# Kernel optimization log

Hardware: AMD Instinct MI355X
Metric: run time of the kernel (lower is better)

## Reference

```python
import jax, jax.numpy as jnp
import numpy as np

SEQ_LEN = 1024
WINDOW = 32
NUM_HEADS = 16
BATCH = 8
DIM = 1024


def make_local_mask(seq_len=SEQ_LEN, window=WINDOW):
    # True = position is MASKED (disallowed), matching the torch bool attn_mask.
    # torch allows j in [i - window//2, i + window//2] inclusive.
    i = np.arange(seq_len)[:, None]
    j = np.arange(seq_len)[None, :]
    half = window // 2
    allowed = (j >= i - half) & (j <= i + half)
    return jnp.asarray(~allowed)


def setup_inputs() -> dict:
    key = jax.random.key(0)
    k_x, k_wi, k_wo = jax.random.split(key, 3)
    scale_in = 1.0 / np.sqrt(DIM)
    return {
        "x": jax.random.normal(k_x, (BATCH, SEQ_LEN, DIM), dtype=jnp.float32),
        "w_in": jax.random.normal(k_wi, (3 * DIM, DIM), dtype=jnp.float32) * scale_in,
        "b_in": jnp.zeros((3 * DIM,), dtype=jnp.float32),
        "w_out": jax.random.normal(k_wo, (DIM, DIM), dtype=jnp.float32) * scale_in,
        "b_out": jnp.zeros((DIM,), dtype=jnp.float32),
        "mask": make_local_mask(),
    }


def reference(x, w_in, b_in, w_out, b_out, mask):
    B, S, D = x.shape
    H = NUM_HEADS
    hd = D // H
    # fused in-projection (torch nn.MultiheadAttention self-attn path)
    qkv = x @ w_in.T + b_in                      # [B, S, 3D]
    q, k, v = jnp.split(qkv, 3, axis=-1)
    q = q.reshape(B, S, H, hd).transpose(0, 2, 1, 3)  # [B, H, S, hd]
    k = k.reshape(B, S, H, hd).transpose(0, 2, 1, 3)
    v = v.reshape(B, S, H, hd).transpose(0, 2, 1, 3)
    scores = jnp.einsum("bhqd,bhkd->bhqk", q, k) / jnp.sqrt(jnp.asarray(hd, x.dtype))
    neg = jnp.asarray(jnp.finfo(x.dtype).min, x.dtype)
    scores = jnp.where(mask[None, None, :, :], neg, scores)
    attn = jax.nn.softmax(scores, axis=-1)
    ctx = jnp.einsum("bhqk,bhkd->bhqd", attn, v)  # [B, H, S, hd]
    ctx = ctx.transpose(0, 2, 1, 3).reshape(B, S, D)
    return ctx @ w_out.T + b_out
```

## Files before the change

kernel.cpp:

```cpp
#include <hip/hip_runtime.h>

#define S_LEN   1024
#define NH      16
#define HD      64
#define BATCHN  8
#define DMODEL  1024
#define HALF_W  16

typedef __attribute__((ext_vector_type(8))) short bf16x8;
typedef __attribute__((ext_vector_type(4))) float f32x4;

__device__ __forceinline__ unsigned short f2bf(float f) {
  unsigned u = __builtin_bit_cast(unsigned, f);
  u += 0x7fffu + ((u >> 16) & 1u);
  return (unsigned short)(u >> 16);
}
__device__ __forceinline__ float bf2f(unsigned short h) {
  return __builtin_bit_cast(float, ((unsigned)h) << 16);
}

__device__ __forceinline__ void gload_lds16(const void* g, void* l) {
  __builtin_amdgcn_global_load_lds(
      (const __attribute__((address_space(1))) void*)g,
      (__attribute__((address_space(3))) void*)l, 16, 0, 0);
}

__global__ __launch_bounds__(256) void cvt_bf16_kernel(
    const float* __restrict__ in, unsigned short* __restrict__ out, int n4) {
  int t = blockIdx.x * 256 + threadIdx.x;
  if (t >= n4) return;
  float4 v = reinterpret_cast<const float4*>(in)[t];
  ushort4 o = make_ushort4(f2bf(v.x), f2bf(v.y), f2bf(v.z), f2bf(v.w));
  reinterpret_cast<ushort4*>(out)[t] = o;
}

#define MFMA_BF16 __builtin_amdgcn_mfma_f32_16x16x32_bf16

template <int OUT_BF16, int CHN>
__global__ __launch_bounds__(512, 2) void gemmdp_kernel(
    const unsigned short* __restrict__ A,
    const unsigned short* __restrict__ B,
    const float* __restrict__ bias,
    void* __restrict__ Cv,
    int N, int gy) {
  __shared__ __align__(16) unsigned short sA[2][2][CHN * 4096];
  __shared__ __align__(16) unsigned short sB[2][2][8192];

  const int tid  = threadIdx.x;
  const int lane = tid & 63;
  const int wid  = tid >> 6;
  const int wm   = wid >> 2;
  const int wn   = wid & 3;
  const int lgrp = lane >> 4;
  const int l15  = lane & 15;

  const int nwg = gridDim.x;
  const int cpx = nwg >> 3;
  const int sid = (blockIdx.x & 7) * cpx + (blockIdx.x >> 3);
  const int tileM = (sid / gy) * (CHN * 128);
  const int tileN = (sid % gy) * 256;

  const int srow = tid >> 2;
  const int scol = ((tid & 3) ^ ((tid >> 3) & 3)) * 8;
  const unsigned short* gA_s = A + (size_t)(tileM + srow) * 1024 + scol;
  const unsigned short* gB_s = B + (size_t)(tileN + srow) * 1024 + scol;

  const int fch  = (lgrp ^ ((l15 >> 1) & 3)) * 8;
  const int arow = (wm * (CHN * 64) + l15) * 32 + fch;
  const int brow = (wn * 64 + l15) * 32 + fch;

  f32x4 acc[CHN * 4][4] = {};
  bf16x8 nb0 = {}, nb1 = {}, nb2 = {}, nb3 = {};

#define SSA(KT, BUF, KH) do {                                              \
    const unsigned short* _sa = gA_s + (KT) * 64 + (KH) * 32;              \
    gload_lds16(_sa, &sA[BUF][KH][wid * 512]);                             \
    if constexpr (CHN == 2)                                                \
      gload_lds16(_sa + 131072, &sA[BUF][KH][4096 + wid * 512]);           \
  } while (0)
#define SSB(KT, BUF, KH) do {                                              \
    const unsigned short* _sb = gB_s + (KT) * 64 + (KH) * 32;              \
    gload_lds16(_sb, &sB[BUF][KH][wid * 512]);                             \
    gload_lds16(_sb + 131072, &sB[BUF][KH][4096 + wid * 512]);             \
  } while (0)

#define GATE_S do {                                                        \
    if constexpr (CHN == 2) asm volatile("s_waitcnt vmcnt(8)" ::: "memory");\
    else                    asm volatile("s_waitcnt vmcnt(6)" ::: "memory");\
    __builtin_amdgcn_sched_barrier(0);                                     \
    __builtin_amdgcn_s_barrier(); } while (0)
#define GATE_H do {                                                        \
    if constexpr (CHN == 2) asm volatile("s_waitcnt vmcnt(4)" ::: "memory");\
    else                    asm volatile("s_waitcnt vmcnt(3)" ::: "memory");\
    __builtin_amdgcn_sched_barrier(0);                                     \
    __builtin_amdgcn_s_barrier(); } while (0)
#define GATE_Z do {                                                        \
    asm volatile("s_waitcnt vmcnt(0)" ::: "memory");                       \
    __builtin_amdgcn_sched_barrier(0);                                     \
    __builtin_amdgcn_s_barrier(); } while (0)

#define PH(BUF, KH, CH, STG) do {                                          \
    const unsigned short* _pa = &sA[BUF][KH][arow + (CH) * 2048];          \
    bf16x8 a0_ = *(const bf16x8*)(_pa);                                    \
    bf16x8 a1_ = *(const bf16x8*)(_pa + 512);                              \
    bf16x8 a2_ = *(const bf16x8*)(_pa + 1024);                             \
    bf16x8 a3_ = *(const bf16x8*)(_pa + 1536);                             \
    if ((CH) == 0) {                                                       \
      const unsigned short* _pb = &sB[BUF][KH][brow];                      \
      nb0 = *(const bf16x8*)(_pb);        nb1 = *(const bf16x8*)(_pb + 512);  \
      nb2 = *(const bf16x8*)(_pb + 1024); nb3 = *(const bf16x8*)(_pb + 1536); } \
    STG;                                                                   \
    asm volatile("s_waitcnt lgkmcnt(0)" ::: "memory");                     \
    __builtin_amdgcn_sched_barrier(0);                                     \
    __builtin_amdgcn_s_setprio(1);                                         \
    acc[(CH)*4+0][0] = MFMA_BF16(a0_, nb0, acc[(CH)*4+0][0], 0, 0, 0);     \
    acc[(CH)*4+0][1] = MFMA_BF16(a0_, nb1, acc[(CH)*4+0][1], 0, 0, 0);     \
    acc[(CH)*4+0][2] = MFMA_BF16(a0_, nb2, acc[(CH)*4+0][2], 0, 0, 0);     \
    acc[(CH)*4+0][3] = MFMA_BF16(a0_, nb3, acc[(CH)*4+0][3], 0, 0, 0);     \
    acc[(CH)*4+1][0] = MFMA_BF16(a1_, nb0, acc[(CH)*4+1][0], 0, 0, 0);     \
    acc[(CH)*4+1][1] = MFMA_BF16(a1_, nb1, acc[(CH)*4+1][1], 0, 0, 0);     \
    acc[(CH)*4+1][2] = MFMA_BF16(a1_, nb2, acc[(CH)*4+1][2], 0, 0, 0);     \
    acc[(CH)*4+1][3] = MFMA_BF16(a1_, nb3, acc[(CH)*4+1][3], 0, 0, 0);     \
    acc[(CH)*4+2][0] = MFMA_BF16(a2_, nb0, acc[(CH)*4+2][0], 0, 0, 0);     \
    acc[(CH)*4+2][1] = MFMA_BF16(a2_, nb1, acc[(CH)*4+2][1], 0, 0, 0);     \
    acc[(CH)*4+2][2] = MFMA_BF16(a2_, nb2, acc[(CH)*4+2][2], 0, 0, 0);     \
    acc[(CH)*4+2][3] = MFMA_BF16(a2_, nb3, acc[(CH)*4+2][3], 0, 0, 0);     \
    acc[(CH)*4+3][0] = MFMA_BF16(a3_, nb0, acc[(CH)*4+3][0], 0, 0, 0);     \
    acc[(CH)*4+3][1] = MFMA_BF16(a3_, nb1, acc[(CH)*4+3][1], 0, 0, 0);     \
    acc[(CH)*4+3][2] = MFMA_BF16(a3_, nb2, acc[(CH)*4+3][2], 0, 0, 0);     \
    acc[(CH)*4+3][3] = MFMA_BF16(a3_, nb3, acc[(CH)*4+3][3], 0, 0, 0);     \
    __builtin_amdgcn_s_setprio(0);                                         \
  } while (0)

#define DOPAIR(BUF, KH, STGA, STGB) do {                                   \
    if constexpr (CHN == 2) {                                              \
      PH(BUF, KH, 0, STGA);                                                \
      PH(BUF, KH, 1, STGB);                                                \
    } else {                                                               \
      PH(BUF, KH, 0, do { STGA; STGB; } while (0));                        \
    } } while (0)
#define NOSTG ((void)0)

  SSA(0, 0, 0); SSB(0, 0, 0);
  SSA(0, 0, 1); SSB(0, 0, 1);
  SSA(1, 1, 0); SSB(1, 1, 0);

#pragma unroll 1
  for (int kt = 0; kt < 14; kt += 2) {
    GATE_S; DOPAIR(0, 0, SSA(kt + 1, 1, 1), SSB(kt + 1, 1, 1));
    GATE_S; DOPAIR(0, 1, SSA(kt + 2, 0, 0), SSB(kt + 2, 0, 0));
    GATE_S; DOPAIR(1, 0, SSA(kt + 2, 0, 1), SSB(kt + 2, 0, 1));
    GATE_S; DOPAIR(1, 1, SSA(kt + 3, 1, 0), SSB(kt + 3, 1, 0));
  }
  GATE_S; DOPAIR(0, 0, SSA(15, 1, 1), SSB(15, 1, 1));
  GATE_S; DOPAIR(0, 1, NOSTG, NOSTG);
  GATE_H; DOPAIR(1, 0, NOSTG, NOSTG);
  GATE_Z; DOPAIR(1, 1, NOSTG, NOSTG);

#undef SSA
#undef SSB
#undef GATE_S
#undef GATE_H
#undef GATE_Z
#undef PH
#undef DOPAIR
#undef NOSTG

#pragma unroll
  for (int nt = 0; nt < 4; ++nt) {
    const int col = tileN + wn * 64 + nt * 16 + l15;
    const float bs = bias[col];
#pragma unroll
    for (int ch = 0; ch < CHN; ++ch)
#pragma unroll
      for (int mt = 0; mt < 4; ++mt) {
        const int row0 = tileM + wm * (CHN * 64) + ch * 64 + mt * 16 + lgrp * 4;
#pragma unroll
        for (int rr = 0; rr < 4; ++rr) {
          float v = acc[ch * 4 + mt][nt][rr] + bs;
          if (OUT_BF16) {
            ((unsigned short*)Cv)[(size_t)(row0 + rr) * N + col] = f2bf(v);
          } else {
            ((float*)Cv)[(size_t)(row0 + rr) * N + col] = v;
          }
        }
      }
  }
}

#define KST 72
#define PST 104

__global__ __launch_bounds__(256) void attn_local_kernel(
    const unsigned short* __restrict__ qkv, unsigned short* __restrict__ ctx) {
  __shared__ __align__(16) unsigned short sKP[96 * KST];
  __shared__ __align__(16) unsigned short sQ[64 * KST];
  __shared__ __align__(16) unsigned short sVT[64 * PST];

  const int tid  = threadIdx.x;
  const int lane = tid & 63;
  const int wid  = tid >> 6;
  const int qc   = lane & 15;
  const int lgrp = lane >> 4;

  const int qb = blockIdx.x & 15;
  const int h  = (blockIdx.x >> 4) & 15;
  const int b  = blockIdx.x >> 8;
  const int i0 = qb * 64;

  const unsigned short* hb = qkv + (size_t)b * S_LEN * 3072 + (size_t)h * HD;

#pragma unroll
  for (int it = 0; it < 3; ++it) {
    int c  = it * 256 + tid;
    int r  = c >> 3;
    int d0 = (c & 7) * 8;
    int j  = i0 - 16 + r;
    bf16x8 kv = {}, vv = {};
    if (0 <= j && j < S_LEN) {
      const unsigned short* rp = hb + (size_t)j * 3072;
      kv = *reinterpret_cast<const bf16x8*>(rp + DMODEL + d0);
      vv = *reinterpret_cast<const bf16x8*>(rp + 2 * DMODEL + d0);
    }
    *reinterpret_cast<bf16x8*>(&sKP[r * KST + d0]) = kv;
#pragma unroll
    for (int jj = 0; jj < 8; ++jj) {
      int dd = (jj + c) & 7;
      sVT[(d0 + dd) * PST + r] = (unsigned short)vv[dd];
    }
  }
#pragma unroll
  for (int it = 0; it < 2; ++it) {
    int c  = it * 256 + tid;
    int r  = c >> 3;
    int d0 = (c & 7) * 8;
    bf16x8 qv = *reinterpret_cast<const bf16x8*>(hb + (size_t)(i0 + r) * 3072 + d0);
    *reinterpret_cast<bf16x8*>(&sQ[r * KST + d0]) = qv;
  }
  __syncthreads();

  const int q0 = wid * 16;

  bf16x8 bq[2];
#pragma unroll
  for (int ks = 0; ks < 2; ++ks)
    bq[ks] = *reinterpret_cast<const bf16x8*>(
        &sQ[(q0 + qc) * KST + ks * 32 + lgrp * 8]);

  f32x4 st[6] = {};
#pragma unroll
  for (int kt = 0; kt < 6; ++kt) {
#pragma unroll
    for (int ks = 0; ks < 2; ++ks) {
      bf16x8 fa = *reinterpret_cast<const bf16x8*>(
          &sKP[(kt * 16 + qc) * KST + ks * 32 + lgrp * 8]);
      st[kt] = __builtin_amdgcn_mfma_f32_16x16x32_bf16(fa, bq[ks], st[kt], 0, 0, 0);
    }
  }
  __syncthreads();

  const int q = q0 + qc;
  float pv[6][4];
  float mx = -3.0e38f;
#pragma unroll
  for (int kt = 0; kt < 6; ++kt)
#pragma unroll
    for (int rr = 0; rr < 4; ++rr) {
      int kk = kt * 16 + lgrp * 4 + rr;
      int j  = i0 - 16 + kk;
      bool ok = (j >= 0) && (j < S_LEN) && (kk >= q) && (kk <= q + 32);
      float s = ok ? st[kt][rr] * 0.125f : -3.0e38f;
      pv[kt][rr] = s;
      mx = fmaxf(mx, s);
    }
  mx = fmaxf(mx, __shfl_xor(mx, 16, 64));
  mx = fmaxf(mx, __shfl_xor(mx, 32, 64));

  float rsum = 0.f;
#pragma unroll
  for (int kt = 0; kt < 6; ++kt)
#pragma unroll
    for (int rr = 0; rr < 4; ++rr) {
      float p = __expf(pv[kt][rr] - mx);
      pv[kt][rr] = p;
      rsum += p;
    }
  rsum += __shfl_xor(rsum, 16, 64);
  rsum += __shfl_xor(rsum, 32, 64);
  const float inv = 1.0f / rsum;

  unsigned short* sP = sKP;
#pragma unroll
  for (int kt = 0; kt < 6; ++kt) {
    ushort4 w = make_ushort4(f2bf(pv[kt][0]), f2bf(pv[kt][1]),
                             f2bf(pv[kt][2]), f2bf(pv[kt][3]));
    *reinterpret_cast<ushort4*>(&sP[(q0 + qc) * PST + kt * 16 + lgrp * 4]) = w;
  }

  bf16x8 pb[3];
#pragma unroll
  for (int ks = 0; ks < 3; ++ks)
    pb[ks] = *reinterpret_cast<const bf16x8*>(
        &sP[(q0 + qc) * PST + ks * 32 + lgrp * 8]);

  f32x4 ct[4] = {};
#pragma unroll
  for (int dt = 0; dt < 4; ++dt)
#pragma unroll
    for (int ks = 0; ks < 3; ++ks) {
      bf16x8 fa = *reinterpret_cast<const bf16x8*>(
          &sVT[(dt * 16 + qc) * PST + ks * 32 + lgrp * 8]);
      ct[dt] = __builtin_amdgcn_mfma_f32_16x16x32_bf16(fa, pb[ks], ct[dt], 0, 0, 0);
    }

  unsigned short* op =
      ctx + ((size_t)b * S_LEN + i0 + q0 + qc) * DMODEL + h * HD;
#pragma unroll
  for (int dt = 0; dt < 4; ++dt) {
    ushort4 w = make_ushort4(
        f2bf(ct[dt][0] * inv), f2bf(ct[dt][1] * inv),
        f2bf(ct[dt][2] * inv), f2bf(ct[dt][3] * inv));
    *reinterpret_cast<ushort4*>(op + dt * 16 + lgrp * 4) = w;
  }
}

extern "C" void kernel_launch(void* const* d_in, const int* in_sizes, int n_in,
                              void* d_out, int out_size, void* d_ws, size_t ws_size,
                              hipStream_t stream) {
  const float* x     = (const float*)d_in[0];
  const float* w_in  = (const float*)d_in[1];
  const float* b_in  = (const float*)d_in[2];
  const float* w_out = (const float*)d_in[3];
  const float* b_out = (const float*)d_in[4];
  float* out = (float*)d_out;

  unsigned short* xb   = (unsigned short*)d_ws;
  unsigned short* wib  = xb  + (size_t)8192 * 1024;
  unsigned short* wob  = wib + (size_t)3072 * 1024;
  unsigned short* qkv  = wob + (size_t)1024 * 1024;
  unsigned short* ctxb = qkv + (size_t)8192 * 3072;

  cvt_bf16_kernel<<<8192, 256, 0, stream>>>(x, xb, (8192 * 1024) / 4);
  cvt_bf16_kernel<<<3072, 256, 0, stream>>>(w_in, wib, (3072 * 1024) / 4);
  cvt_bf16_kernel<<<1024, 256, 0, stream>>>(w_out, wob, (1024 * 1024) / 4);

  gemmdp_kernel<1, 2><<<384, 512, 0, stream>>>(
      xb, wib, b_in, (void*)qkv, 3072, 12);

  attn_local_kernel<<<BATCHN * NH * (S_LEN / 64), 256, 0, stream>>>(qkv, ctxb);

  gemmdp_kernel<0, 1><<<256, 512, 0, stream>>>(
      ctxb, wob, b_out, (void*)out, 1024, 4);
}
```

Baseline: 128.3 us.

## Retile QKV projection GEMM to 256x384 tiles with 4-stage LDS ring

The in-projection GEMM gets a dedicated kernel. Each workgroup computes a 256x384 tile, giving 256 workgroups (one per CU) instead of 384. K is streamed in 32-wide steps through a 4-slot LDS ring, with loads issued three steps ahead. This aims to remove the partial second wave and raise operand reuse per LDS load. In exchange it needs 48 accumulators per lane and 160KB of LDS, which limits occupancy and adds register pressure. The out-projection GEMM is specialised with its constants, with no structural change.

New measurement: 121.2 us. 5.6% less time.

```diff
diff --git a/kernel.cpp b/kernel.cpp
--- a/kernel.cpp
+++ b/kernel.cpp
@@ -36,15 +36,12 @@
 
 #define MFMA_BF16 __builtin_amdgcn_mfma_f32_16x16x32_bf16
 
-template <int OUT_BF16, int CHN>
-__global__ __launch_bounds__(512, 2) void gemmdp_kernel(
+__global__ __launch_bounds__(512, 2) void gemm_inproj_kernel(
     const unsigned short* __restrict__ A,
     const unsigned short* __restrict__ B,
     const float* __restrict__ bias,
-    void* __restrict__ Cv,
-    int N, int gy) {
-  __shared__ __align__(16) unsigned short sA[2][2][CHN * 4096];
-  __shared__ __align__(16) unsigned short sB[2][2][8192];
+    unsigned short* __restrict__ C) {
+  __shared__ __align__(16) unsigned short lds[81920];
 
   const int tid  = threadIdx.x;
   const int lane = tid & 63;
@@ -54,11 +51,9 @@
   const int lgrp = lane >> 4;
   const int l15  = lane & 15;
 
-  const int nwg = gridDim.x;
-  const int cpx = nwg >> 3;
-  const int sid = (blockIdx.x & 7) * cpx + (blockIdx.x >> 3);
-  const int tileM = (sid / gy) * (CHN * 128);
-  const int tileN = (sid % gy) * 256;
+  const int sid = (blockIdx.x & 7) * 32 + (blockIdx.x >> 3);
+  const int tileM = (sid >> 3) * 256;
+  const int tileN = (sid & 7) * 384;
 
   const int srow = tid >> 2;
   const int scol = ((tid & 3) ^ ((tid >> 3) & 3)) * 8;
@@ -66,79 +61,184 @@
   const unsigned short* gB_s = B + (size_t)(tileN + srow) * 1024 + scol;
 
   const int fch  = (lgrp ^ ((l15 >> 1) & 3)) * 8;
-  const int arow = (wm * (CHN * 64) + l15) * 32 + fch;
+  const int arow = (wm * 128 + l15) * 32 + fch;
+  const int brow = (wn * 96 + l15) * 32 + fch;
+
+  f32x4 acc[48] = {};
+
+#define STG(S) do { const int _q = (S) & 3;                                \
+    const unsigned short* _ga = gA_s + (S) * 32;                           \
+    const unsigned short* _gb = gB_s + (S) * 32;                           \
+    gload_lds16(_ga,          &lds[_q * 8192 + tid * 8]);                  \
+    gload_lds16(_ga + 131072, &lds[_q * 8192 + 4096 + tid * 8]);           \
+    gload_lds16(_gb,          &lds[32768 + _q * 12288 + tid * 8]);         \
+    gload_lds16(_gb + 131072, &lds[32768 + _q * 12288 + 4096 + tid * 8]);  \
+    gload_lds16(_gb + 262144, &lds[32768 + _q * 12288 + 8192 + tid * 8]);  \
+  } while (0)
+
+#define M24(MB)                                                            \
+    acc[(MB+0)*6+0] = MFMA_BF16(a0_, b0_, acc[(MB+0)*6+0], 0, 0, 0);       \
+    acc[(MB+0)*6+1] = MFMA_BF16(a0_, b1_, acc[(MB+0)*6+1], 0, 0, 0);       \
+    acc[(MB+0)*6+2] = MFMA_BF16(a0_, b2_, acc[(MB+0)*6+2], 0, 0, 0);       \
+    acc[(MB+0)*6+3] = MFMA_BF16(a0_, b3_, acc[(MB+0)*6+3], 0, 0, 0);       \
+    acc[(MB+0)*6+4] = MFMA_BF16(a0_, b4_, acc[(MB+0)*6+4], 0, 0, 0);       \
+    acc[(MB+0)*6+5] = MFMA_BF16(a0_, b5_, acc[(MB+0)*6+5], 0, 0, 0);       \
+    acc[(MB+1)*6+0] = MFMA_BF16(a1_, b0_, acc[(MB+1)*6+0], 0, 0, 0);       \
+    acc[(MB+1)*6+1] = MFMA_BF16(a1_, b1_, acc[(MB+1)*6+1], 0, 0, 0);       \
+    acc[(MB+1)*6+2] = MFMA_BF16(a1_, b2_, acc[(MB+1)*6+2], 0, 0, 0);       \
+    acc[(MB+1)*6+3] = MFMA_BF16(a1_, b3_, acc[(MB+1)*6+3], 0, 0, 0);       \
+    acc[(MB+1)*6+4] = MFMA_BF16(a1_, b4_, acc[(MB+1)*6+4], 0, 0, 0);       \
+    acc[(MB+1)*6+5] = MFMA_BF16(a1_, b5_, acc[(MB+1)*6+5], 0, 0, 0);       \
+    acc[(MB+2)*6+0] = MFMA_BF16(a2_, b0_, acc[(MB+2)*6+0], 0, 0, 0);       \
+    acc[(MB+2)*6+1] = MFMA_BF16(a2_, b1_, acc[(MB+2)*6+1], 0, 0, 0);       \
+    acc[(MB+2)*6+2] = MFMA_BF16(a2_, b2_, acc[(MB+2)*6+2], 0, 0, 0);       \
+    acc[(MB+2)*6+3] = MFMA_BF16(a2_, b3_, acc[(MB+2)*6+3], 0, 0, 0);       \
+    acc[(MB+2)*6+4] = MFMA_BF16(a2_, b4_, acc[(MB+2)*6+4], 0, 0, 0);       \
+    acc[(MB+2)*6+5] = MFMA_BF16(a2_, b5_, acc[(MB+2)*6+5], 0, 0, 0);       \
+    acc[(MB+3)*6+0] = MFMA_BF16(a3_, b0_, acc[(MB+3)*6+0], 0, 0, 0);       \
+    acc[(MB+3)*6+1] = MFMA_BF16(a3_, b1_, acc[(MB+3)*6+1], 0, 0, 0);       \
+    acc[(MB+3)*6+2] = MFMA_BF16(a3_, b2_, acc[(MB+3)*6+2], 0, 0, 0);       \
+    acc[(MB+3)*6+3] = MFMA_BF16(a3_, b3_, acc[(MB+3)*6+3], 0, 0, 0);       \
+    acc[(MB+3)*6+4] = MFMA_BF16(a3_, b4_, acc[(MB+3)*6+4], 0, 0, 0);       \
+    acc[(MB+3)*6+5] = MFMA_BF16(a3_, b5_, acc[(MB+3)*6+5], 0, 0, 0);
+
+  STG(0); STG(1); STG(2);
+
+#pragma unroll 1
+  for (int p = 0; p < 32; ++p) {
+    if (p < 30)       { asm volatile("s_waitcnt vmcnt(10)" ::: "memory"); }
+    else if (p == 30) { asm volatile("s_waitcnt vmcnt(5)"  ::: "memory"); }
+    else              { asm volatile("s_waitcnt vmcnt(0)"  ::: "memory"); }
+    __builtin_amdgcn_sched_barrier(0);
+    __builtin_amdgcn_s_barrier();
+
+    if (p <= 28) STG(p + 3);
+
+    const int slot = p & 3;
+    const unsigned short* pa = &lds[slot * 8192 + arow];
+    const unsigned short* pb = &lds[32768 + slot * 12288 + brow];
+
+    bf16x8 b0_ = *(const bf16x8*)(pb);
+    bf16x8 b1_ = *(const bf16x8*)(pb + 512);
+    bf16x8 b2_ = *(const bf16x8*)(pb + 1024);
+    bf16x8 b3_ = *(const bf16x8*)(pb + 1536);
+    bf16x8 b4_ = *(const bf16x8*)(pb + 2048);
+    bf16x8 b5_ = *(const bf16x8*)(pb + 2560);
+    bf16x8 a0_ = *(const bf16x8*)(pa);
+    bf16x8 a1_ = *(const bf16x8*)(pa + 512);
+    bf16x8 a2_ = *(const bf16x8*)(pa + 1024);
+    bf16x8 a3_ = *(const bf16x8*)(pa + 1536);
+    asm volatile("s_waitcnt lgkmcnt(0)" ::: "memory");
+    __builtin_amdgcn_sched_barrier(0);
+    __builtin_amdgcn_s_setprio(1);
+    M24(0)
+    __builtin_amdgcn_s_setprio(0);
+
+    a0_ = *(const bf16x8*)(pa + 2048);
+    a1_ = *(const bf16x8*)(pa + 2560);
+    a2_ = *(const bf16x8*)(pa + 3072);
+    a3_ = *(const bf16x8*)(pa + 3584);
+    asm volatile("s_waitcnt lgkmcnt(0)" ::: "memory");
+    __builtin_amdgcn_sched_barrier(0);
+    __builtin_amdgcn_s_setprio(1);
+    M24(4)
+    __builtin_amdgcn_s_setprio(0);
+  }
+#undef STG
+#undef M24
+
+#pragma unroll
+  for (int nt = 0; nt < 6; ++nt) {
+    const int col = tileN + wn * 96 + nt * 16 + l15;
+    const float bs = bias[col];
+#pragma unroll
+    for (int mt = 0; mt < 8; ++mt) {
+      const int row0 = tileM + wm * 128 + mt * 16 + lgrp * 4;
+#pragma unroll
+      for (int rr = 0; rr < 4; ++rr)
+        C[(size_t)(row0 + rr) * 3072 + col] = f2bf(acc[mt * 6 + nt][rr] + bs);
+    }
+  }
+}
+
+__global__ __launch_bounds__(512, 2) void gemm_outproj_kernel(
+    const unsigned short* __restrict__ A,
+    const unsigned short* __restrict__ B,
+    const float* __restrict__ bias,
+    float* __restrict__ Cv) {
+  __shared__ __align__(16) unsigned short sA[2][2][4096];
+  __shared__ __align__(16) unsigned short sB[2][2][8192];
+
+  const int tid  = threadIdx.x;
+  const int lane = tid & 63;
+  const int wid  = tid >> 6;
+  const int wm   = wid >> 2;
+  const int wn   = wid & 3;
+  const int lgrp = lane >> 4;
+  const int l15  = lane & 15;
+
+  const int sid = (blockIdx.x & 7) * 32 + (blockIdx.x >> 3);
+  const int tileM = (sid >> 2) * 128;
+  const int tileN = (sid & 3) * 256;
+
+  const int srow = tid >> 2;
+  const int scol = ((tid & 3) ^ ((tid >> 3) & 3)) * 8;
+  const unsigned short* gA_s = A + (size_t)(tileM + srow) * 1024 + scol;
+  const unsigned short* gB_s = B + (size_t)(tileN + srow) * 1024 + scol;
+
+  const int fch  = (lgrp ^ ((l15 >> 1) & 3)) * 8;
+  const int arow = (wm * 64 + l15) * 32 + fch;
   const int brow = (wn * 64 + l15) * 32 + fch;
 
-  f32x4 acc[CHN * 4][4] = {};
-  bf16x8 nb0 = {}, nb1 = {}, nb2 = {}, nb3 = {};
+  f32x4 acc[4][4] = {};
 
 #define SSA(KT, BUF, KH) do {                                              \
-    const unsigned short* _sa = gA_s + (KT) * 64 + (KH) * 32;              \
-    gload_lds16(_sa, &sA[BUF][KH][wid * 512]);                             \
-    if constexpr (CHN == 2)                                                \
-      gload_lds16(_sa + 131072, &sA[BUF][KH][4096 + wid * 512]);           \
+    gload_lds16(gA_s + (KT) * 64 + (KH) * 32, &sA[BUF][KH][wid * 512]);    \
   } while (0)
 #define SSB(KT, BUF, KH) do {                                              \
     const unsigned short* _sb = gB_s + (KT) * 64 + (KH) * 32;              \
-    gload_lds16(_sb, &sB[BUF][KH][wid * 512]);                             \
+    gload_lds16(_sb,          &sB[BUF][KH][wid * 512]);                    \
     gload_lds16(_sb + 131072, &sB[BUF][KH][4096 + wid * 512]);             \
   } while (0)
 
-#define GATE_S do {                                                        \
-    if constexpr (CHN == 2) asm volatile("s_waitcnt vmcnt(8)" ::: "memory");\
-    else                    asm volatile("s_waitcnt vmcnt(6)" ::: "memory");\
+#define GATE(NSTR) do {                                                    \
+    asm volatile("s_waitcnt vmcnt(" NSTR ")" ::: "memory");                \
     __builtin_amdgcn_sched_barrier(0);                                     \
     __builtin_amdgcn_s_barrier(); } while (0)
-#define GATE_H do {                                                        \
-    if constexpr (CHN == 2) asm volatile("s_waitcnt vmcnt(4)" ::: "memory");\
-    else                    asm volatile("s_waitcnt vmcnt(3)" ::: "memory");\
-    __builtin_amdgcn_sched_barrier(0);                                     \
-    __builtin_amdgcn_s_barrier(); } while (0)
-#define GATE_Z do {                                                        \
-    asm volatile("s_waitcnt vmcnt(0)" ::: "memory");                       \
-    __builtin_amdgcn_sched_barrier(0);                                     \
-    __builtin_amdgcn_s_barrier(); } while (0)
-
-#define PH(BUF, KH, CH, STG) do {                                          \
-    const unsigned short* _pa = &sA[BUF][KH][arow + (CH) * 2048];          \
+
+#define PH1(BUF, KH, STGA, STGB) do {                                      \
+    STGA; STGB;                                                            \
+    const unsigned short* _pa = &sA[BUF][KH][arow];                        \
+    const unsigned short* _pb = &sB[BUF][KH][brow];                        \
     bf16x8 a0_ = *(const bf16x8*)(_pa);                                    \
     bf16x8 a1_ = *(const bf16x8*)(_pa + 512);                              \
     bf16x8 a2_ = *(const bf16x8*)(_pa + 1024);                             \
     bf16x8 a3_ = *(const bf16x8*)(_pa + 1536);                             \
-    if ((CH) == 0) {                                                       \
-      const unsigned short* _pb = &sB[BUF][KH][brow];                      \
-      nb0 = *(const bf16x8*)(_pb);        nb1 = *(const bf16x8*)(_pb + 512);  \
-      nb2 = *(const bf16x8*)(_pb + 1024); nb3 = *(const bf16x8*)(_pb + 1536); } \
-    STG;                                                                   \
+    bf16x8 nb0 = *(const bf16x8*)(_pb);                                    \
+    bf16x8 nb1 = *(const bf16x8*)(_pb + 512);                              \
+    bf16x8 nb2 = *(const bf16x8*)(_pb + 1024);                             \
+    bf16x8 nb3 = *(const bf16x8*)(_pb + 1536);                             \
     asm volatile("s_waitcnt lgkmcnt(0)" ::: "memory");                     \
     __builtin_amdgcn_sched_barrier(0);                                     \
     __builtin_amdgcn_s_setprio(1);                                         \
-    acc[(CH)*4+0][0] = MFMA_BF16(a0_, nb0, acc[(CH)*4+0][0], 0, 0, 0);     \
-    acc[(CH)*4+0][1] = MFMA_BF16(a0_, nb1, acc[(CH)*4+0][1], 0, 0, 0);     \
-    acc[(CH)*4+0][2] = MFMA_BF16(a0_, nb2, acc[(CH)*4+0][2], 0, 0, 0);     \
-    acc[(CH)*4+0][3] = MFMA_BF16(a0_, nb3, acc[(CH)*4+0][3], 0, 0, 0);     \
-    acc[(CH)*4+1][0] = MFMA_BF16(a1_, nb0, acc[(CH)*4+1][0], 0, 0, 0);     \
-    acc[(CH)*4+1][1] = MFMA_BF16(a1_, nb1, acc[(CH)*4+1][1], 0, 0, 0);     \
-    acc[(CH)*4+1][2] = MFMA_BF16(a1_, nb2, acc[(CH)*4+1][2], 0, 0, 0);     \
-    acc[(CH)*4+1][3] = MFMA_BF16(a1_, nb3, acc[(CH)*4+1][3], 0, 0, 0);     \
-    acc[(CH)*4+2][0] = MFMA_BF16(a2_, nb0, acc[(CH)*4+2][0], 0, 0, 0);     \
-    acc[(CH)*4+2][1] = MFMA_BF16(a2_, nb1, acc[(CH)*4+2][1], 0, 0, 0);     \
-    acc[(CH)*4+2][2] = MFMA_BF16(a2_, nb2, acc[(CH)*4+2][2], 0, 0, 0);     \
-    acc[(CH)*4+2][3] = MFMA_BF16(a2_, nb3, acc[(CH)*4+2][3], 0, 0, 0);     \
-    acc[(CH)*4+3][0] = MFMA_BF16(a3_, nb0, acc[(CH)*4+3][0], 0, 0, 0);     \
-    acc[(CH)*4+3][1] = MFMA_BF16(a3_, nb1, acc[(CH)*4+3][1], 0, 0, 0);     \
-    acc[(CH)*4+3][2] = MFMA_BF16(a3_, nb2, acc[(CH)*4+3][2], 0, 0, 0);     \
-    acc[(CH)*4+3][3] = MFMA_BF16(a3_, nb3, acc[(CH)*4+3][3], 0, 0, 0);     \
+    acc[0][0] = MFMA_BF16(a0_, nb0, acc[0][0], 0, 0, 0);                   \
+    acc[0][1] = MFMA_BF16(a0_, nb1, acc[0][1], 0, 0, 0);                   \
+    acc[0][2] = MFMA_BF16(a0_, nb2, acc[0][2], 0, 0, 0);                   \
+    acc[0][3] = MFMA_BF16(a0_, nb3, acc[0][3], 0, 0, 0);                   \
+    acc[1][0] = MFMA_BF16(a1_, nb0, acc[1][0], 0, 0, 0);                   \
+    acc[1][1] = MFMA_BF16(a1_, nb1, acc[1][1], 0, 0, 0);                   \
+    acc[1][2] = MFMA_BF16(a1_, nb2, acc[1][2], 0, 0, 0);                   \
+    acc[1][3] = MFMA_BF16(a1_, nb3, acc[1][3], 0, 0, 0);                   \
+    acc[2][0] = MFMA_BF16(a2_, nb0, acc[2][0], 0, 0, 0);                   \
+    acc[2][1] = MFMA_BF16(a2_, nb1, acc[2][1], 0, 0, 0);                   \
+    acc[2][2] = MFMA_BF16(a2_, nb2, acc[2][2], 0, 0, 0);                   \
+    acc[2][3] = MFMA_BF16(a2_, nb3, acc[2][3], 0, 0, 0);                   \
+    acc[3][0] = MFMA_BF16(a3_, nb0, acc[3][0], 0, 0, 0);                   \
+    acc[3][1] = MFMA_BF16(a3_, nb1, acc[3][1], 0, 0, 0);                   \
+    acc[3][2] = MFMA_BF16(a3_, nb2, acc[3][2], 0, 0, 0);                   \
+    acc[3][3] = MFMA_BF16(a3_, nb3, acc[3][3], 0, 0, 0);                   \
     __builtin_amdgcn_s_setprio(0);                                         \
   } while (0)
-
-#define DOPAIR(BUF, KH, STGA, STGB) do {                                   \
-    if constexpr (CHN == 2) {                                              \
-      PH(BUF, KH, 0, STGA);                                                \
-      PH(BUF, KH, 1, STGB);                                                \
-    } else {                                                               \
-      PH(BUF, KH, 0, do { STGA; STGB; } while (0));                        \
-    } } while (0)
 #define NOSTG ((void)0)
 
   SSA(0, 0, 0); SSB(0, 0, 0);
@@ -147,23 +247,20 @@
 
 #pragma unroll 1
   for (int kt = 0; kt < 14; kt += 2) {
-    GATE_S; DOPAIR(0, 0, SSA(kt + 1, 1, 1), SSB(kt + 1, 1, 1));
-    GATE_S; DOPAIR(0, 1, SSA(kt + 2, 0, 0), SSB(kt + 2, 0, 0));
-    GATE_S; DOPAIR(1, 0, SSA(kt + 2, 0, 1), SSB(kt + 2, 0, 1));
-    GATE_S; DOPAIR(1, 1, SSA(kt + 3, 1, 0), SSB(kt + 3, 1, 0));
-  }
-  GATE_S; DOPAIR(0, 0, SSA(15, 1, 1), SSB(15, 1, 1));
-  GATE_S; DOPAIR(0, 1, NOSTG, NOSTG);
-  GATE_H; DOPAIR(1, 0, NOSTG, NOSTG);
-  GATE_Z; DOPAIR(1, 1, NOSTG, NOSTG);
+    GATE("6"); PH1(0, 0, SSA(kt + 1, 1, 1), SSB(kt + 1, 1, 1));
+    GATE("6"); PH1(0, 1, SSA(kt + 2, 0, 0), SSB(kt + 2, 0, 0));
+    GATE("6"); PH1(1, 0, SSA(kt + 2, 0, 1), SSB(kt + 2, 0, 1));
+    GATE("6"); PH1(1, 1, SSA(kt + 3, 1, 0), SSB(kt + 3, 1, 0));
+  }
+  GATE("6"); PH1(0, 0, SSA(15, 1, 1), SSB(15, 1, 1));
+  GATE("6"); PH1(0, 1, NOSTG, NOSTG);
+  GATE("3"); PH1(1, 0, NOSTG, NOSTG);
+  GATE("0"); PH1(1, 1, NOSTG, NOSTG);
 
 #undef SSA
 #undef SSB
-#undef GATE_S
-#undef GATE_H
-#undef GATE_Z
-#undef PH
-#undef DOPAIR
+#undef GATE
+#undef PH1
 #undef NOSTG
 
 #pragma unroll
@@ -171,20 +268,12 @@
     const int col = tileN + wn * 64 + nt * 16 + l15;
     const float bs = bias[col];
 #pragma unroll
-    for (int ch = 0; ch < CHN; ++ch)
-#pragma unroll
-      for (int mt = 0; mt < 4; ++mt) {
-        const int row0 = tileM + wm * (CHN * 64) + ch * 64 + mt * 16 + lgrp * 4;
-#pragma unroll
-        for (int rr = 0; rr < 4; ++rr) {
-          float v = acc[ch * 4 + mt][nt][rr] + bs;
-          if (OUT_BF16) {
-            ((unsigned short*)Cv)[(size_t)(row0 + rr) * N + col] = f2bf(v);
-          } else {
-            ((float*)Cv)[(size_t)(row0 + rr) * N + col] = v;
-          }
-        }
-      }
+    for (int mt = 0; mt < 4; ++mt) {
+      const int row0 = tileM + wm * 64 + mt * 16 + lgrp * 4;
+#pragma unroll
+      for (int rr = 0; rr < 4; ++rr)
+        Cv[(size_t)(row0 + rr) * 1024 + col] = acc[mt][nt][rr] + bs;
+    }
   }
 }
 
@@ -344,11 +433,9 @@
   cvt_bf16_kernel<<<3072, 256, 0, stream>>>(w_in, wib, (3072 * 1024) / 4);
   cvt_bf16_kernel<<<1024, 256, 0, stream>>>(w_out, wob, (1024 * 1024) / 4);
 
-  gemmdp_kernel<1, 2><<<384, 512, 0, stream>>>(
-      xb, wib, b_in, (void*)qkv, 3072, 12);
+  gemm_inproj_kernel<<<256, 512, 0, stream>>>(xb, wib, b_in, qkv);
 
   attn_local_kernel<<<BATCHN * NH * (S_LEN / 64), 256, 0, stream>>>(qkv, ctxb);
 
-  gemmdp_kernel<0, 1><<<256, 512, 0, stream>>>(
-      ctxb, wob, b_out, (void*)out, 1024, 4);
-}
+  gemm_outproj_kernel<<<256, 512, 0, stream>>>(ctxb, wob, b_out, out);
+}
```
